# Optimization experiments

Hardware: AMD Instinct MI355X
Metric: run time of the kernel (lower is better)

## Reference

```python
import jax, jax.numpy as jnp
import numpy as np

B, N = 16384, 4096
PERCENT_ON = 0.1
TEMPERATURE = 10.0  # training-mode temperature
K = int(round(N * PERCENT_ON))  # 410


def setup_inputs() -> dict:
    key = jax.random.key(0)
    k1, k2 = jax.random.split(key)
    x = jax.random.normal(k1, (B, N), dtype=jnp.float32)
    # Gumbel noise for sampling-without-replacement (Gumbel-top-k trick),
    # equivalent to torch.multinomial(softmax(x/T), k, replacement=False).
    gumbel = jax.random.gumbel(k2, (B, N), dtype=jnp.float32)
    return {"x": x, "gumbel": gumbel}


def reference(x, gumbel):
    # logits with temperature
    logits = x / TEMPERATURE
    # entropy of the categorical distribution per row, averaged (single stable pass)
    logp = jax.nn.log_softmax(logits, axis=-1)
    entropy = jnp.mean(-jnp.sum(jnp.exp(logp) * logp, axis=-1))
    # sample K winners without replacement via Gumbel-top-k
    _, idx = jax.lax.top_k(logits + gumbel, K)  # idx: [B, K]
    rows = jnp.arange(x.shape[0])[:, None]       # [B, 1]
    mask = jnp.zeros_like(x).at[rows, idx].set(1.0)
    out = x * mask  # relu=False path
    return out, entropy
```

## Files before the change

### kernel.cpp

```cpp
#include <hip/hip_runtime.h>
#include <math.h>

#define TPB 256
#define EPT 16
#define NN  4096
#define KSEL 410

__device__ __forceinline__ unsigned sortkey(float f) {
    unsigned u = __float_as_uint(f);
    unsigned m = (unsigned)(((int)u) >> 31);
    return u ^ (m | 0x80000000u);
}

template <bool USE_WS>
__global__ __launch_bounds__(TPB)
void skw_main(const float* __restrict__ x, const float* __restrict__ g,
              float* __restrict__ out, float* __restrict__ rowH,
              float* __restrict__ entAcc, float invB)
{
    const int row  = blockIdx.x;
    const int t    = threadIdx.x;
    const int w    = t >> 6;
    const int lane = t & 63;
    const size_t rbase = (size_t)row * NN;

    float    xv[EPT];
    unsigned key[EPT];
    unsigned bp[EPT / 4];

    __shared__ unsigned hist0[256][9];
    __shared__ unsigned histr[4][256];
    __shared__ unsigned wtot[4];
    __shared__ unsigned wtA[4], wtB[4];
    __shared__ float    fred[8];
    __shared__ unsigned sh_digit, sh_above;

    const float4* xp = reinterpret_cast<const float4*>(x + rbase);
    const float4* gp = reinterpret_cast<const float4*>(g + rbase);
    float4*       op = reinterpret_cast<float4*>(out + rbase);

    float sZ = 0.f, sZL = 0.f;
#pragma unroll
    for (int q = 0; q < EPT / 4; ++q) {
        float4 xx = xp[(q << 8) + t];
        float4 gg = gp[(q << 8) + t];
        float xa[4] = {xx.x, xx.y, xx.z, xx.w};
        float ga[4] = {gg.x, gg.y, gg.z, gg.w};
        unsigned pk = 0;
#pragma unroll
        for (int jj = 0; jj < 4; ++jj) {
            float xs = xa[jj];
            xv[4 * q + jj] = xs;
            float l = xs * 0.1f;
            float e = __expf(l);
            sZ  += e;
            sZL += e * l;
            float q10 = __builtin_fmaf(__builtin_fmaf(-10.0f, l, xs), 0.1f, l);
            float s = q10 + ga[jj];
            key[4 * q + jj] = sortkey(s);
            int b = (int)__builtin_fmaf(s, 16.0f, 64.0f);
            b = min(max(b, 0), 255);
            pk |= (unsigned)b << (8 * jj);
        }
        bp[q] = pk;
    }

#pragma unroll
    for (int sft = 32; sft >= 1; sft >>= 1) { sZ += __shfl_xor(sZ, sft); sZL += __shfl_xor(sZL, sft); }
    if (lane == 0) { fred[w] = sZ; fred[4 + w] = sZL; }

    unsigned* h0 = &hist0[0][0];
#pragma unroll
    for (int i = 0; i < 9; ++i) h0[t + 256 * i] = 0;
    __syncthreads();

    if (t == 0) {
        float Z = fred[0] + fred[1] + fred[2] + fred[3];
        float L = fred[4] + fred[5] + fred[6] + fred[7];
        float H = __logf(Z) - L / Z;
        if (USE_WS) rowH[row] = H;
        else atomicAdd(entAcc, H * invB);
    }

#pragma unroll
    for (int q = 0; q < EPT / 4; ++q) {
        unsigned pk = bp[q];
#pragma unroll
        for (int jj = 0; jj < 4; ++jj)
            atomicAdd(&hist0[(pk >> (8 * jj)) & 255u][lane & 7], 1u);
    }
    __syncthreads();

    unsigned v = 0;
#pragma unroll
    for (int k = 0; k < 8; ++k) v += hist0[t][k];
#pragma unroll
    for (int sft = 1; sft < 64; sft <<= 1) {
        unsigned tmp = __shfl(v, lane + sft);
        v += (lane + sft < 64) ? tmp : 0u;
    }
    if (lane == 0) wtot[w] = v;
    unsigned vnext = __shfl(v, lane + 1);
    __syncthreads();
    unsigned Kr = KSEL;
    {
        unsigned hi = 0;
#pragma unroll
        for (int c = 0; c < 4; ++c) hi += (c > w) ? wtot[c] : 0u;
        unsigned cum     = v + hi;
        unsigned cumNext = ((lane < 63) ? vnext : 0u) + hi;
        if (cum >= Kr && cumNext < Kr) { sh_digit = (unsigned)t; sh_above = cumNext; }
    }
    __syncthreads();
    const unsigned Bstar = sh_digit;
    Kr -= sh_above;

    unsigned cm = 0;
#pragma unroll
    for (int q = 0; q < EPT / 4; ++q) {
        unsigned pk = bp[q];
#pragma unroll
        for (int jj = 0; jj < 4; ++jj)
            cm |= (((pk >> (8 * jj)) & 255u) == Bstar) ? (1u << (4 * q + jj)) : 0u;
    }

    unsigned prefix = 0;
#pragma unroll
    for (int p = 0; p < 4; ++p) {
        const int shift = 24 - 8 * p;
        histr[w][lane] = 0; histr[w][lane + 64] = 0; histr[w][lane + 128] = 0; histr[w][lane + 192] = 0;
#pragma unroll
        for (int j = 0; j < EPT; ++j) {
            if ((cm >> j) & 1u) {
                unsigned k = key[j];
                if (p == 0 || (k >> (shift + 8)) == prefix)
                    atomicAdd(&histr[w][(k >> shift) & 255u], 1u);
            }
        }
        __syncthreads();
        unsigned vv = histr[0][t] + histr[1][t] + histr[2][t] + histr[3][t];
#pragma unroll
        for (int sft = 1; sft < 64; sft <<= 1) {
            unsigned tmp = __shfl(vv, lane + sft);
            vv += (lane + sft < 64) ? tmp : 0u;
        }
        if (lane == 0) wtot[w] = vv;
        unsigned vvn = __shfl(vv, lane + 1);
        __syncthreads();
        unsigned hi2 = 0;
#pragma unroll
        for (int c = 0; c < 4; ++c) hi2 += (c > w) ? wtot[c] : 0u;
        unsigned cum2  = vv + hi2;
        unsigned cumN2 = ((lane < 63) ? vvn : 0u) + hi2;
        if (cum2 >= Kr && cumN2 < Kr) { sh_digit = (unsigned)t; sh_above = cumN2; }
        __syncthreads();
        prefix = (prefix << 8) | sh_digit;
        Kr -= sh_above;
    }
    const unsigned thr = prefix;

    unsigned eq[4];
#pragma unroll
    for (int q = 0; q < 4; ++q) {
        unsigned e = 0;
#pragma unroll
        for (int jj = 0; jj < 4; ++jj) e += (key[4 * q + jj] == thr) ? 1u : 0u;
        eq[q] = e;
    }
    unsigned wA = eq[0] | (eq[1] << 16);
    unsigned wB = eq[2] | (eq[3] << 16);
    unsigned sA = wA, sB = wB;
#pragma unroll
    for (int sft = 1; sft < 64; sft <<= 1) {
        unsigned ta = __shfl(sA, lane - sft);
        unsigned tb = __shfl(sB, lane - sft);
        if (lane >= sft) { sA += ta; sB += tb; }
    }
    if (lane == 63) { wtA[w] = sA; wtB[w] = sB; }
    __syncthreads();
    unsigned offA = 0, offB = 0, totA = 0, totB = 0;
#pragma unroll
    for (int c = 0; c < 4; ++c) {
        totA += wtA[c]; totB += wtB[c];
        if (c < w) { offA += wtA[c]; offB += wtB[c]; }
    }
    unsigned exA = offA + sA - wA;
    unsigned exB = offB + sB - wB;
    unsigned tot0 = totA & 0xFFFFu, tot1 = totA >> 16, tot2 = totB & 0xFFFFu;
    unsigned baseq[4] = {0u, tot0, tot0 + tot1, tot0 + tot1 + tot2};
    unsigned exq[4]   = {exA & 0xFFFFu, exA >> 16, exB & 0xFFFFu, exB >> 16};

#pragma unroll
    for (int q = 0; q < EPT / 4; ++q) {
        unsigned pos = baseq[q] + exq[q];
        float vals[4];
#pragma unroll
        for (int jj = 0; jj < 4; ++jj) {
            int j = 4 * q + jj;
            bool sel;
            if (key[j] > thr)       sel = true;
            else if (key[j] == thr) { sel = (pos < Kr); ++pos; }
            else                    sel = false;
            vals[jj] = sel ? xv[j] : 0.0f;
        }
        float4 o4; o4.x = vals[0]; o4.y = vals[1]; o4.z = vals[2]; o4.w = vals[3];
        op[(q << 8) + t] = o4;
    }
}

__global__ void skw_zero(float* p) { *p = 0.0f; }

__global__ void skw_reduce(const float* __restrict__ rowH, float* __restrict__ outp, int B)
{
    __shared__ float red[256];
    int t = threadIdx.x;
    float s = 0.f;
    for (int i = t; i < B; i += 256) s += rowH[i];
    red[t] = s; __syncthreads();
    for (int st = 128; st > 0; st >>= 1) { if (t < st) red[t] += red[t + st]; __syncthreads(); }
    if (t == 0) *outp = red[0] / (float)B;
}

extern "C" void kernel_launch(void* const* d_in, const int* in_sizes, int n_in,
                              void* d_out, int out_size, void* d_ws, size_t ws_size,
                              hipStream_t stream)
{
    const float* x = (const float*)d_in[0];
    const float* g = (const float*)d_in[1];
    float* out = (float*)d_out;
    const int BN = in_sizes[0];
    const int B  = BN / NN;
    float* entp = out + (size_t)BN;

    if (ws_size >= (size_t)B * sizeof(float)) {
        float* rowH = (float*)d_ws;
        skw_main<true><<<B, TPB, 0, stream>>>(x, g, out, rowH, nullptr, 0.f);
        skw_reduce<<<1, 256, 0, stream>>>(rowH, entp, B);
    } else {
        skw_zero<<<1, 1, 0, stream>>>(entp);
        skw_main<false><<<B, TPB, 0, stream>>>(x, g, out, nullptr, entp, 1.0f / (float)B);
    }
}
```

Before: 170.7 us.

## Replace 4-pass radix refinement with rank-counting over compacted candidate bucket

After the coarse 256-bin histogram picks the bucket holding the K-th element, the candidate keys in that bucket are compacted into shared memory. Each candidate's rank is then computed by brute-force comparison against the others, which locates the exact threshold and the number of ties to take. This replaces four rounds of radix histogramming, each with several block barriers. Output stores are also made nontemporal. The shared list is capped at 1024 entries, so a bucket holding more candidates than that would give a wrong threshold, and the rank search costs O(M^2) work.

```diff
diff --git a/kernel.cpp b/kernel.cpp
--- a/kernel.cpp
+++ b/kernel.cpp
@@ -5,6 +5,9 @@
 #define EPT 16
 #define NN  4096
 #define KSEL 410
+#define CAP 1024
+
+typedef float floatx4 __attribute__((ext_vector_type(4)));
 
 __device__ __forceinline__ unsigned sortkey(float f) {
     unsigned u = __float_as_uint(f);
@@ -29,15 +32,16 @@
     unsigned bp[EPT / 4];
 
     __shared__ unsigned hist0[256][9];
-    __shared__ unsigned histr[4][256];
     __shared__ unsigned wtot[4];
     __shared__ unsigned wtA[4], wtB[4];
     __shared__ float    fred[8];
-    __shared__ unsigned sh_digit, sh_above;
+    __shared__ unsigned sh_digit, sh_above, sh_cnt, sh_thr, sh_take;
+
+    unsigned* list = &hist0[0][0];
 
     const float4* xp = reinterpret_cast<const float4*>(x + rbase);
     const float4* gp = reinterpret_cast<const float4*>(g + rbase);
-    float4*       op = reinterpret_cast<float4*>(out + rbase);
+    floatx4*      op = reinterpret_cast<floatx4*>(out + rbase);
 
     float sZ = 0.f, sZL = 0.f;
 #pragma unroll
@@ -54,7 +58,7 @@
             float l = xs * 0.1f;
             float e = __expf(l);
             sZ  += e;
-            sZL += e * l;
+            sZL = __builtin_fmaf(e, l, sZL);
             float q10 = __builtin_fmaf(__builtin_fmaf(-10.0f, l, xs), 0.1f, l);
             float s = q10 + ga[jj];
             key[4 * q + jj] = sortkey(s);
@@ -72,6 +76,7 @@
     unsigned* h0 = &hist0[0][0];
 #pragma unroll
     for (int i = 0; i < 9; ++i) h0[t + 256 * i] = 0;
+    if (t == 0) sh_cnt = 0;
     __syncthreads();
 
     if (t == 0) {
@@ -123,41 +128,29 @@
         for (int jj = 0; jj < 4; ++jj)
             cm |= (((pk >> (8 * jj)) & 255u) == Bstar) ? (1u << (4 * q + jj)) : 0u;
     }
-
-    unsigned prefix = 0;
-#pragma unroll
-    for (int p = 0; p < 4; ++p) {
-        const int shift = 24 - 8 * p;
-        histr[w][lane] = 0; histr[w][lane + 64] = 0; histr[w][lane + 128] = 0; histr[w][lane + 192] = 0;
-#pragma unroll
-        for (int j = 0; j < EPT; ++j) {
-            if ((cm >> j) & 1u) {
-                unsigned k = key[j];
-                if (p == 0 || (k >> (shift + 8)) == prefix)
-                    atomicAdd(&histr[w][(k >> shift) & 255u], 1u);
-            }
-        }
-        __syncthreads();
-        unsigned vv = histr[0][t] + histr[1][t] + histr[2][t] + histr[3][t];
-#pragma unroll
-        for (int sft = 1; sft < 64; sft <<= 1) {
-            unsigned tmp = __shfl(vv, lane + sft);
-            vv += (lane + sft < 64) ? tmp : 0u;
-        }
-        if (lane == 0) wtot[w] = vv;
-        unsigned vvn = __shfl(vv, lane + 1);
-        __syncthreads();
-        unsigned hi2 = 0;
-#pragma unroll
-        for (int c = 0; c < 4; ++c) hi2 += (c > w) ? wtot[c] : 0u;
-        unsigned cum2  = vv + hi2;
-        unsigned cumN2 = ((lane < 63) ? vvn : 0u) + hi2;
-        if (cum2 >= Kr && cumN2 < Kr) { sh_digit = (unsigned)t; sh_above = cumN2; }
-        __syncthreads();
-        prefix = (prefix << 8) | sh_digit;
-        Kr -= sh_above;
-    }
-    const unsigned thr = prefix;
+#pragma unroll
+    for (int j = 0; j < EPT; ++j) {
+        if ((cm >> j) & 1u) {
+            unsigned p = atomicAdd(&sh_cnt, 1u);
+            if (p < CAP) list[p] = key[j];
+        }
+    }
+    __syncthreads();
+
+    const unsigned M = sh_cnt;
+    for (unsigned i = t; i < M; i += TPB) {
+        unsigned ki = list[i];
+        unsigned gt = 0, eqc = 0;
+        for (unsigned j2 = 0; j2 < M; ++j2) {
+            unsigned kj = list[j2];
+            gt  += (kj > ki) ? 1u : 0u;
+            eqc += (kj == ki) ? 1u : 0u;
+        }
+        if (gt < Kr && Kr <= gt + eqc) { sh_thr = ki; sh_take = Kr - gt; }
+    }
+    __syncthreads();
+    const unsigned thr    = sh_thr;
+    const unsigned KrTake = sh_take;
 
     unsigned eq[4];
 #pragma unroll
@@ -199,12 +192,13 @@
             int j = 4 * q + jj;
             bool sel;
             if (key[j] > thr)       sel = true;
-            else if (key[j] == thr) { sel = (pos < Kr); ++pos; }
+            else if (key[j] == thr) { sel = (pos < KrTake); ++pos; }
             else                    sel = false;
             vals[jj] = sel ? xv[j] : 0.0f;
         }
-        float4 o4; o4.x = vals[0]; o4.y = vals[1]; o4.z = vals[2]; o4.w = vals[3];
-        op[(q << 8) + t] = o4;
+        floatx4 o4;
+        o4.x = vals[0]; o4.y = vals[1]; o4.z = vals[2]; o4.w = vals[3];
+        __builtin_nontemporal_store(o4, &op[(q << 8) + t]);
     }
 }
 
```

Result: faster. 166.9 us (-2.3%).
